# Kernel optimization log

Hardware: AMD Instinct MI355X
Metric: run time of the kernel (lower is better)

## Reference

```python
import jax, jax.numpy as jnp
import numpy as np

B, C, IMG, P = 64, 3, 224, 16
HP = IMG // P                 # 14 patches per side
N = HP * HP                   # 196 patches
R = 196                       # num_superpixels
D, HEADS, DEPTH = 384, 6, 12
HD = D // HEADS
MLP = 4 * D
CLS = 1000
WIN = 4                       # local attention window radius
SEQ = R + 1


def setup_inputs() -> dict:
    key = jax.random.key(0)
    ks = jax.random.split(key, 16)
    nrm = lambda k, s: jax.random.normal(k, s, jnp.float32) * 0.02
    return dict(
        x=jax.random.normal(ks[0], (B, C, IMG, IMG), jnp.float32),
        seg=jax.random.randint(ks[1], (B, IMG, IMG), 0, R, jnp.int32),
        patch_W=nrm(ks[2], (C * P * P, D)), patch_b=jnp.zeros((D,), jnp.float32),
        cls_token=nrm(ks[3], (1, 1, D)),
        pos_W=nrm(ks[4], (2, D)), pos_b=jnp.zeros((D,), jnp.float32),
        cls_pos=nrm(ks[5], (D,)),
        ln1_w=jnp.ones((DEPTH, D), jnp.float32), ln1_b=jnp.zeros((DEPTH, D), jnp.float32),
        qkv_W=nrm(ks[6], (DEPTH, D, 3 * D)), qkv_b=jnp.zeros((DEPTH, 3 * D), jnp.float32),
        proj_W=nrm(ks[7], (DEPTH, D, D)), proj_b=jnp.zeros((DEPTH, D), jnp.float32),
        ln2_w=jnp.ones((DEPTH, D), jnp.float32), ln2_b=jnp.zeros((DEPTH, D), jnp.float32),
        mlp_W1=nrm(ks[8], (DEPTH, D, MLP)), mlp_b1=jnp.zeros((DEPTH, MLP), jnp.float32),
        mlp_W2=nrm(ks[9], (DEPTH, MLP, D)), mlp_b2=jnp.zeros((DEPTH, D), jnp.float32),
        norm_w=jnp.ones((D,), jnp.float32), norm_b=jnp.zeros((D,), jnp.float32),
        head_W=nrm(ks[10], (D, CLS)), head_b=jnp.zeros((CLS,), jnp.float32),
    )


def _ln(x, w, b):
    m = x.mean(-1, keepdims=True)
    v = ((x - m) ** 2).mean(-1, keepdims=True)
    return (x - m) * jax.lax.rsqrt(v + 1e-5) * w + b


def _forward(x, seg, patch_W, patch_b, cls_token, pos_W, pos_b, cls_pos,
             ln1_w, ln1_b, qkv_W, qkv_b, proj_W, proj_b, ln2_w, ln2_b,
             mlp_W1, mlp_b1, mlp_W2, mlp_b2, norm_w, norm_b, head_W, head_b):
    # --- patch embedding (conv stride==kernel == patchify + matmul) -> [B,N,D]
    xp = x.reshape(B, C, HP, P, HP, P).transpose(0, 2, 4, 1, 3, 5).reshape(B, N, C * P * P)
    emb = xp @ patch_W + patch_b
    # --- patch -> superpixel id: segmentation label at patch center pixel
    centers = jnp.arange(HP) * P + P // 2
    patch_seg = seg[:, centers[:, None], centers[None, :]].reshape(B, N)
    # --- mean pooling per superpixel (fused segment reduce over all batches)
    pids = (jnp.arange(B, dtype=patch_seg.dtype)[:, None] * R + patch_seg).reshape(-1)
    sums = jax.ops.segment_sum(emb.reshape(-1, D), pids, num_segments=B * R)
    cnts = jax.ops.segment_sum(jnp.ones((B * N,), emb.dtype), pids, num_segments=B * R)
    pooled = (sums / jnp.maximum(cnts, 1.0)[:, None]).reshape(B, R, D)
    # --- superpixel centroids via pixel-level segment reduce -> [B,R,2] (x,y)
    coords = jnp.arange(IMG, dtype=jnp.float32) / IMG
    yg, xg = jnp.meshgrid(coords, coords, indexing='ij')
    gid = (jnp.arange(B, dtype=seg.dtype)[:, None] * R + seg.reshape(B, -1)).reshape(-1)
    pix = IMG * IMG
    pcnt = jax.ops.segment_sum(jnp.ones((B * pix,), jnp.float32), gid, num_segments=B * R)
    ysum = jax.ops.segment_sum(jnp.broadcast_to(yg.reshape(-1), (B, pix)).reshape(-1), gid, num_segments=B * R)
    xsum = jax.ops.segment_sum(jnp.broadcast_to(xg.reshape(-1), (B, pix)).reshape(-1), gid, num_segments=B * R)
    safe = jnp.maximum(pcnt, 1.0)
    cx = jnp.where(pcnt > 0, xsum / safe, 0.5)
    cy = jnp.where(pcnt > 0, ysum / safe, 0.5)
    centroids = jnp.stack([cx, cy], axis=-1).reshape(B, R, 2)
    # --- prepend cls token, add dynamic (centroid-based) positional encoding
    tok = jnp.concatenate([jnp.broadcast_to(cls_token, (B, 1, D)), pooled], axis=1)
    pos = jnp.concatenate([jnp.broadcast_to(cls_pos[None, None, :], (B, 1, D)),
                           centroids @ pos_W + pos_b], axis=1)
    h = tok + pos
    # --- local (banded) attention mask; cls token attends globally
    idx = jnp.arange(SEQ)
    band = jnp.abs(idx[:, None] - idx[None, :]) <= WIN
    band = band | (idx[:, None] == 0) | (idx[None, :] == 0)
    neg = jnp.float32(-1e9)
    scale = 1.0 / np.sqrt(HD)
    for l in range(DEPTH):
        z = _ln(h, ln1_w[l], ln1_b[l])
        qkv = (z @ qkv_W[l] + qkv_b[l]).reshape(B, SEQ, 3, HEADS, HD)
        q, k, v = qkv[:, :, 0], qkv[:, :, 1], qkv[:, :, 2]
        s = jnp.einsum('bqhd,bkhd->bhqk', q, k) * scale
        s = jnp.where(band[None, None], s, neg)
        a = jax.nn.softmax(s, axis=-1)
        o = jnp.einsum('bhqk,bkhd->bqhd', a, v).reshape(B, SEQ, D)
        h = h + o @ proj_W[l] + proj_b[l]
        z = _ln(h, ln2_w[l], ln2_b[l])
        h = h + jax.nn.gelu(z @ mlp_W1[l] + mlp_b1[l]) @ mlp_W2[l] + mlp_b2[l]
    h = _ln(h, norm_w, norm_b)
    return h[:, 0] @ head_W + head_b


def reference(x, seg, patch_W, patch_b, cls_token, pos_W, pos_b, cls_pos,
              ln1_w, ln1_b, qkv_W, qkv_b, proj_W, proj_b, ln2_w, ln2_b,
              mlp_W1, mlp_b1, mlp_W2, mlp_b2, norm_w, norm_b, head_W, head_b):
    return _forward(x, seg, patch_W, patch_b, cls_token, pos_W, pos_b, cls_pos,
                    ln1_w, ln1_b, qkv_W, qkv_b, proj_W, proj_b, ln2_w, ln2_b,
                    mlp_W1, mlp_b1, mlp_W2, mlp_b2, norm_w, norm_b, head_W, head_b)
```

## Files before the change

### kernel.cpp

```cpp
#include <hip/hip_runtime.h>
#include <hip/hip_bf16.h>
#include <math.h>

typedef unsigned short ushort_t;
typedef unsigned int uint_t;
typedef __attribute__((ext_vector_type(8))) short short8;
typedef __attribute__((ext_vector_type(4))) float f32x4;

#define BATCH 64
#define CHN 3
#define IMG 224
#define PATCH 16
#define HP 14
#define NPATCH 196
#define RSEG 196
#define DMODEL 384
#define HEADS 6
#define HD 64
#define DEPTH 12
#define MLPD 1536
#define CLS 1000
#define WIN 4
#define SEQ 197
#define PIX (IMG*IMG)
#define PATCHK (CHN*PATCH*PATCH)
#define CPARTS 16
#define PPP (PIX / CPARTS)

__device__ __forceinline__ ushort_t f2bf(float f) {
  uint_t u = __float_as_uint(f);
  u += 0x7FFFu + ((u >> 16) & 1u);
  return (ushort_t)(u >> 16);
}
__device__ __forceinline__ float bf2f(ushort_t u) {
  return __uint_as_float((uint_t)u << 16);
}
__device__ __forceinline__ float gelu_tanh(float x) {
  float z = 0.7978845608028654f * (x + 0.044715f * x * x * x);
  z = fminf(fmaxf(z, -15.f), 15.f);
  float t = exp2f(2.8853900817779268f * z);
  return x * t / (t + 1.f);
}
__device__ __forceinline__ int xcd_swizzle(int bid, int nwg) {
  int q = nwg >> 3, r = nwg & 7;
  int xcd = bid & 7, idx = bid >> 3;
  int start = (xcd < r) ? xcd * (q + 1) : r * (q + 1) + (xcd - r) * q;
  return start + idx;
}
__device__ __forceinline__ float dot16bf(const ushort_t* a, const ushort_t* b) {
  const uint_t* a32 = (const uint_t*)a;
  const uint_t* b32 = (const uint_t*)b;
  float acc = 0.f;
#pragma unroll
  for (int w = 0; w < 8; w++) {
    uint_t ka = a32[w], kb = b32[w];
    acc += bf2f((ushort_t)(ka & 0xffff)) * bf2f((ushort_t)(kb & 0xffff));
    acc += bf2f((ushort_t)(ka >> 16)) * bf2f((ushort_t)(kb >> 16));
  }
  return acc;
}

__global__ __launch_bounds__(256) void convtrans_kernel(
    const float* __restrict__ W, ushort_t* __restrict__ Wt, int K, int N) {
  __shared__ float t[32][33];
  int k0 = blockIdx.y * 32, n0 = blockIdx.x * 32;
  const float* Wl = W + (size_t)blockIdx.z * K * N;
  ushort_t* Wtl = Wt + (size_t)blockIdx.z * K * N;
  int tx = threadIdx.x & 31, ty = threadIdx.x >> 5;
#pragma unroll
  for (int i = 0; i < 32; i += 8)
    t[ty + i][tx] = Wl[(size_t)(k0 + ty + i) * N + n0 + tx];
  __syncthreads();
#pragma unroll
  for (int i = 0; i < 32; i += 8)
    Wtl[(size_t)(n0 + ty + i) * K + k0 + tx] = f2bf(t[tx][ty + i]);
}

__global__ __launch_bounds__(256) void patchify_kernel(
    const float* __restrict__ x, ushort_t* __restrict__ xp, int total4) {
  int idx = blockIdx.x * 256 + threadIdx.x;
  if (idx >= total4) return;
  int kq = idx % (PATCHK / 4);
  int m = idx / (PATCHK / 4);
  int n = m % NPATCH;
  int b = m / NPATCH;
  int hi = n / HP, wi = n % HP;
  int k = kq * 4;
  int c = k >> 8;
  int rem = k & 255;
  int pi = rem >> 4, pj = rem & 15;
  int row = hi * PATCH + pi, col = wi * PATCH + pj;
  f32x4 v = *(const f32x4*)&x[(((size_t)b * CHN + c) * IMG + row) * IMG + col];
  uint_t p0 = (uint_t)f2bf(v[0]) | ((uint_t)f2bf(v[1]) << 16);
  uint_t p1 = (uint_t)f2bf(v[2]) | ((uint_t)f2bf(v[3]) << 16);
  uint_t* dst = (uint_t*)(xp + (size_t)idx * 4);
  dst[0] = p0;
  dst[1] = p1;
}

template <int BMT, bool GELU, bool RESID, int OUTMODE>
__global__ __launch_bounds__(256) void gemm_gl(
    const ushort_t* __restrict__ A, const ushort_t* __restrict__ Bt,
    const float* __restrict__ bias, const float* __restrict__ resid,
    void* __restrict__ Cout, int M, int N, int K, int gx) {
  constexpr int AWS = BMT * 2;
  constexpr int AI = AWS / 64;
  constexpr int MF = 4;
  constexpr int NF = (BMT == 128) ? 4 : 2;
  constexpr int BUF_U = (BMT + 128) * 64;
  constexpr int CS_U = BMT * 136;
  constexpr int SMEM_U = (2 * BUF_U > CS_U) ? 2 * BUF_U : CS_U;
  __shared__ __align__(16) ushort_t smem[SMEM_U];
  int tid = threadIdx.x;
  int wave = tid >> 6, lane = tid & 63;
  int flat = xcd_swizzle(blockIdx.x, gridDim.x);
  int bx = flat % gx, by = flat / gx;
  int bm = by * BMT, bn = bx * 128;
  int wr = (BMT == 128) ? (wave >> 1) * 64 : 0;
  int wc = (BMT == 128) ? (wave & 1) * 64 : wave * 32;
  f32x4 acc[MF][NF];
#pragma unroll
  for (int m = 0; m < MF; m++)
#pragma unroll
    for (int n = 0; n < NF; n++)
#pragma unroll
      for (int e = 0; e < 4; e++) acc[m][n][e] = 0.f;

  int r = lane & 15;
  int cfrag = lane >> 4;

  const ushort_t* asrc[AI];
  uint_t adst[AI];
#pragma unroll
  for (int j = 0; j < AI; j++) {
    int s = wave * AWS + j * 64 + lane;
    int row = s >> 3;
    int cp = s & 7;
    int c = cp ^ ((row >> 1) & 7);
    asrc[j] = A + (size_t)(bm + row) * K + c * 8;
    adst[j] = (uint_t)(wave * AWS + j * 64) * 8;
  }
  const ushort_t* bsrc[4];
  uint_t bdst[4];
#pragma unroll
  for (int j = 0; j < 4; j++) {
    int s = wave * 256 + j * 64 + lane;
    int row = s >> 3;
    int cp = s & 7;
    int c = cp ^ ((row >> 1) & 7);
    bsrc[j] = Bt + (size_t)(bn + row) * K + c * 8;
    bdst[j] = (uint_t)(BMT * 64) + (uint_t)(wave * 256 + j * 64) * 8;
  }
  uint_t aoff[2][MF], boff[2][NF];
#pragma unroll
  for (int kk = 0; kk < 2; kk++) {
#pragma unroll
    for (int m = 0; m < MF; m++) {
      int row = wr + m * 16 + r;
      int sl = (kk * 4 + cfrag) ^ ((row >> 1) & 7);
      aoff[kk][m] = (uint_t)(row * 64 + sl * 8);
    }
#pragma unroll
    for (int n = 0; n < NF; n++) {
      int row = wc + n * 16 + r;
      int sl = (kk * 4 + cfrag) ^ ((row >> 1) & 7);
      boff[kk][n] = (uint_t)(BMT * 64 + row * 64 + sl * 8);
    }
  }

  auto STAGE = [&](int buf) {
    ushort_t* base = smem + buf * BUF_U;
#pragma unroll
    for (int j = 0; j < AI; j++)
      __builtin_amdgcn_global_load_lds(
          (const __attribute__((address_space(1))) void*)asrc[j],
          (__attribute__((address_space(3))) void*)(base + adst[j]), 16, 0, 0);
#pragma unroll
    for (int j = 0; j < 4; j++)
      __builtin_amdgcn_global_load_lds(
          (const __attribute__((address_space(1))) void*)bsrc[j],
          (__attribute__((address_space(3))) void*)(base + bdst[j]), 16, 0, 0);
  };
  auto ADVANCE = [&]() {
#pragma unroll
    for (int j = 0; j < AI; j++) asrc[j] += 64;
#pragma unroll
    for (int j = 0; j < 4; j++) bsrc[j] += 64;
  };

  STAGE(0);
  ADVANCE();
  __syncthreads();
  int cur = 0;
  for (int k0 = 0; k0 < K; k0 += 64) {
    if (k0 + 64 < K) {
      STAGE(cur ^ 1);
      ADVANCE();
    }
    ushort_t* base = smem + cur * BUF_U;
#pragma unroll
    for (int kk = 0; kk < 2; kk++) {
      short8 af[MF], bfr[NF];
#pragma unroll
      for (int m = 0; m < MF; m++)
        af[m] = *(const short8*)(base + aoff[kk][m]);
#pragma unroll
      for (int n = 0; n < NF; n++)
        bfr[n] = *(const short8*)(base + boff[kk][n]);
      __builtin_amdgcn_s_setprio(1);
#pragma unroll
      for (int m = 0; m < MF; m++)
#pragma unroll
        for (int n = 0; n < NF; n++)
          acc[m][n] = __builtin_amdgcn_mfma_f32_16x16x32_bf16(
              af[m], bfr[n], acc[m][n], 0, 0, 0);
      __builtin_amdgcn_s_setprio(0);
    }
    __syncthreads();
    cur ^= 1;
  }
  int q4 = (lane >> 4) * 4;
  if (OUTMODE == 0) {
#pragma unroll
    for (int n = 0; n < NF; n++) {
      int col = bn + wc + n * 16 + r;
      float bi = bias[col];
#pragma unroll
      for (int m = 0; m < MF; m++) {
#pragma unroll
        for (int e = 0; e < 4; e++) {
          int row = bm + wr + m * 16 + q4 + e;
          if (row < M) {
            float v = acc[m][n][e] + bi;
            if (GELU) v = gelu_tanh(v);
            if (RESID) v += resid[(size_t)row * N + col];
            ((float*)Cout)[(size_t)row * N + col] = v;
          }
        }
      }
    }
  } else {
    ushort_t* Cs = smem;
#pragma unroll
    for (int n = 0; n < NF; n++) {
      int lc = wc + n * 16 + r;
      float bi = bias[bn + lc];
#pragma unroll
      for (int m = 0; m < MF; m++) {
#pragma unroll
        for (int e = 0; e < 4; e++) {
          int lr = wr + m * 16 + q4 + e;
          float v = acc[m][n][e] + bi;
          if (GELU) v = gelu_tanh(v);
          if (RESID) v += resid[(size_t)(bm + lr) * N + bn + lc];
          Cs[lr * 136 + lc] = f2bf(v);
        }
      }
    }
    __syncthreads();
    constexpr int CHUNKS = BMT * 16;
#pragma unroll
    for (int c = 0; c < CHUNKS / 256; c++) {
      int id = c * 256 + tid;
      int row = id >> 4, ch = id & 15;
      int grow = bm + row;
      if (grow < M) {
        short8 val = *(const short8*)(Cs + row * 136 + ch * 8);
        int gcol = bn + ch * 8;
        if (OUTMODE == 1) {
          *(short8*)((ushort_t*)Cout + (size_t)grow * N + gcol) = val;
        } else {
          int b_ = grow / SEQ, t_ = grow - b_ * SEQ;
          int which = gcol / DMODEL;
          int hcol = gcol - which * DMODEL;
          int hh = hcol >> 6, d0 = hcol & 63;
          *(short8*)((ushort_t*)Cout +
                     ((((size_t)b_ * 3 + which) * HEADS + hh) * SEQ + t_) * 64 +
                     d0) = val;
        }
      }
    }
  }
}

__global__ __launch_bounds__(256) void zeroacc_kernel(int* __restrict__ g,
                                                      int n) {
  int i = blockIdx.x * 256 + threadIdx.x;
  if (i < n) g[i] = 0;
}

__global__ __launch_bounds__(256) void centroid_part_kernel(
    const int* __restrict__ seg, int* __restrict__ gacc) {
  __shared__ int cnt[RSEG], si[RSEG], sj[RSEG];
  int b = blockIdx.x, part = blockIdx.y, tid = threadIdx.x;
  for (int r = tid; r < RSEG; r += 256) { cnt[r] = 0; si[r] = 0; sj[r] = 0; }
  __syncthreads();
  const int* s = seg + (size_t)b * PIX;
  int p0 = part * PPP;
  for (int p = p0 + tid; p < p0 + PPP; p += 256) {
    int r = s[p];
    int i = p / IMG, j = p % IMG;
    atomicAdd(&cnt[r], 1);
    atomicAdd(&si[r], i);
    atomicAdd(&sj[r], j);
  }
  __syncthreads();
  for (int r = tid; r < RSEG; r += 256) {
    int c = cnt[r];
    if (c | si[r] | sj[r]) {
      int* g = gacc + ((size_t)b * RSEG + r) * 3;
      atomicAdd(&g[0], c);
      atomicAdd(&g[1], si[r]);
      atomicAdd(&g[2], sj[r]);
    }
  }
}
__global__ __launch_bounds__(256) void centroid_fin_kernel(
    const int* __restrict__ gacc, float* __restrict__ cent) {
  int b = blockIdx.x, tid = threadIdx.x;
  for (int r = tid; r < RSEG; r += 256) {
    const int* g = gacc + ((size_t)b * RSEG + r) * 3;
    int c = g[0];
    float cx = 0.5f, cy = 0.5f;
    if (c > 0) {
      cx = ((float)g[2] / (float)IMG) / (float)c;
      cy = ((float)g[1] / (float)IMG) / (float)c;
    }
    cent[((size_t)b * RSEG + r) * 2 + 0] = cx;
    cent[((size_t)b * RSEG + r) * 2 + 1] = cy;
  }
}

__global__ __launch_bounds__(256) void patchseg_kernel(
    const int* __restrict__ seg, int* __restrict__ pseg) {
  int idx = blockIdx.x * 256 + threadIdx.x;
  if (idx >= BATCH * NPATCH) return;
  int n = idx % NPATCH, b = idx / NPATCH;
  int hi = n / HP, wi = n % HP;
  pseg[idx] = seg[(size_t)b * PIX + (8 + hi * PATCH) * IMG + (8 + wi * PATCH)];
}

__global__ __launch_bounds__(64) void buildlists_kernel(
    const int* __restrict__ pseg, int* __restrict__ starts,
    int* __restrict__ lists) {
  __shared__ int cnt[RSEG];
  int b = blockIdx.x;
  if (threadIdx.x != 0) return;
  const int* ps = pseg + b * NPATCH;
  for (int r = 0; r < RSEG; r++) cnt[r] = 0;
  for (int n = 0; n < NPATCH; n++) cnt[ps[n]]++;
  int run = 0;
  int* st = starts + b * (RSEG + 1);
  for (int r = 0; r < RSEG; r++) {
    st[r] = run;
    int c = cnt[r];
    cnt[r] = run;
    run += c;
  }
  st[RSEG] = run;
  int* li = lists + b * NPATCH;
  for (int n = 0; n < NPATCH; n++) {
    int r = ps[n];
    li[cnt[r]++] = n;
  }
}

__global__ __launch_bounds__(384) void pool_assemble_kernel(
    const float* __restrict__ emb, const float* __restrict__ cent,
    const int* __restrict__ starts, const int* __restrict__ lists,
    const float* __restrict__ cls_token, const float* __restrict__ cls_pos,
    const float* __restrict__ pos_W, const float* __restrict__ pos_b,
    float* __restrict__ h) {
  int t = blockIdx.x;
  int b = t / SEQ, s = t % SEQ;
  int d = threadIdx.x;
  float out;
  if (s == 0) {
    out = cls_token[d] + cls_pos[d];
  } else {
    int r = s - 1;
    int st = starts[b * (RSEG + 1) + r];
    int en = starts[b * (RSEG + 1) + r + 1];
    float acc = 0.f;
    for (int i = st; i < en; i++) {
      int n = lists[b * NPATCH + i];
      acc += emb[((size_t)b * NPATCH + n) * DMODEL + d];
    }
    int cnt = en - st;
    float pooled = acc / (float)(cnt > 0 ? cnt : 1);
    float cx = cent[((size_t)b * RSEG + r) * 2 + 0];
    float cy = cent[((size_t)b * RSEG + r) * 2 + 1];
    out = pooled + cx * pos_W[d] + cy * pos_W[DMODEL + d] + pos_b[d];
  }
  h[(size_t)t * DMODEL + d] = out;
}

template <bool OUTBF16>
__global__ __launch_bounds__(256) void ln_kernel(
    const float* __restrict__ in, void* __restrict__ out,
    const float* __restrict__ w, const float* __restrict__ b, int inStride) {
  int wave = threadIdx.x >> 6, lane = threadIdx.x & 63;
  int row = blockIdx.x * 4 + wave;
  const float* xr = in + (size_t)row * inStride;
  float2 v0 = *(const float2*)(xr + lane * 2);
  float2 v1 = *(const float2*)(xr + 128 + lane * 2);
  float2 v2 = *(const float2*)(xr + 256 + lane * 2);
  float s = v0.x + v0.y + v1.x + v1.y + v2.x + v2.y;
  float s2 = v0.x * v0.x + v0.y * v0.y + v1.x * v1.x + v1.y * v1.y +
             v2.x * v2.x + v2.y * v2.y;
#pragma unroll
  for (int off = 32; off; off >>= 1) {
    s += __shfl_xor(s, off);
    s2 += __shfl_xor(s2, off);
  }
  float m = s / (float)DMODEL;
  float var = s2 / (float)DMODEL - m * m;
  float rs = rsqrtf(var + 1e-5f);
#pragma unroll
  for (int i = 0; i < 3; i++) {
    int d0 = i * 128 + lane * 2;
    float x0 = (i == 0) ? v0.x : (i == 1) ? v1.x : v2.x;
    float x1 = (i == 0) ? v0.y : (i == 1) ? v1.y : v2.y;
    float o0 = (x0 - m) * rs * w[d0] + b[d0];
    float o1 = (x1 - m) * rs * w[d0 + 1] + b[d0 + 1];
    if (OUTBF16) {
      uint_t pack = (uint_t)f2bf(o0) | ((uint_t)f2bf(o1) << 16);
      *(uint_t*)((ushort_t*)out + (size_t)row * DMODEL + d0) = pack;
    } else {
      float2 pk = {o0, o1};
      *(float2*)((float*)out + (size_t)row * DMODEL + d0) = pk;
    }
  }
}

__global__ __launch_bounds__(256) void attn_kernel(
    const ushort_t* __restrict__ qkvp, ushort_t* __restrict__ o) {
  int wave = threadIdx.x >> 6, lane = threadIdx.x & 63;
  int gi = blockIdx.x * 4 + wave;
  int hh = blockIdx.y, b = blockIdx.z;
  const size_t hstride = (size_t)HEADS * SEQ * 64;
  size_t base0 = ((size_t)b * 3 * HEADS + hh) * SEQ * 64;
  const ushort_t* Qh = qkvp + base0;
  const ushort_t* Kh = qkvp + base0 + hstride;
  const ushort_t* Vh = qkvp + base0 + 2 * hstride;
  if (gi < 49) {
    int q0 = 1 + gi * 4;
    int base = q0 - 4;
    if (base < 1) base = 1;
    int row = lane >> 2, dq = lane & 3;
    int key = (row == 0) ? 0 : base + row - 1;
    bool rowvalid = (key <= 196);
    int kaddr = rowvalid ? key : 196;
    const uint_t* kp = (const uint_t*)(Kh + (size_t)kaddr * 64 + dq * 16);
    uint_t kf[8];
#pragma unroll
    for (int w = 0; w < 8; w++) kf[w] = kp[w];
    float v[16];
#pragma unroll
    for (int r = 0; r < 16; r++) {
      int kr = (r == 0) ? 0 : base + r - 1;
      if (kr > 196) kr = 196;
      v[r] = bf2f(Vh[(size_t)kr * 64 + lane]);
    }
#pragma unroll
    for (int i = 0; i < 4; i++) {
      int qi = q0 + i;
      const uint_t* qp = (const uint_t*)(Qh + (size_t)qi * 64 + dq * 16);
      float part = 0.f;
#pragma unroll
      for (int w = 0; w < 8; w++) {
        uint_t ka = kf[w], qa = qp[w];
        part += bf2f((ushort_t)(ka & 0xffff)) * bf2f((ushort_t)(qa & 0xffff));
        part += bf2f((ushort_t)(ka >> 16)) * bf2f((ushort_t)(qa >> 16));
      }
      part += __shfl_xor(part, 1);
      part += __shfl_xor(part, 2);
      int lo = qi - WIN;
      if (lo < 1) lo = 1;
      int hi = qi + WIN;
      if (hi > 196) hi = 196;
      bool valid = rowvalid && ((key == 0) || (key >= lo && key <= hi));
      float s = valid ? part * 0.125f : -1e30f;
      float mx = s;
      mx = fmaxf(mx, __shfl_xor(mx, 4));
      mx = fmaxf(mx, __shfl_xor(mx, 8));
      mx = fmaxf(mx, __shfl_xor(mx, 16));
      mx = fmaxf(mx, __shfl_xor(mx, 32));
      float p = valid ? expf(s - mx) : 0.f;
      float sum = p;
      sum += __shfl_xor(sum, 4);
      sum += __shfl_xor(sum, 8);
      sum += __shfl_xor(sum, 16);
      sum += __shfl_xor(sum, 32);
      float acc = 0.f;
#pragma unroll
      for (int r = 0; r < 16; r++) acc += __shfl(p, r * 4) * v[r];
      o[((size_t)(b * SEQ + qi)) * DMODEL + hh * HD + lane] = f2bf(acc / sum);
    }
  } else if (gi == 49) {
    const ushort_t* qr = Qh;
    float sc0 = -1e30f, sc1 = -1e30f, sc2 = -1e30f, sc3 = -1e30f;
#pragma unroll
    for (int c = 0; c < 4; c++) {
      int key = c * 64 + lane;
      float s = -1e30f;
      if (key < SEQ) {
        const ushort_t* kr = Kh + (size_t)key * 64;
        float acc = dot16bf(kr, qr) + dot16bf(kr + 16, qr + 16) +
                    dot16bf(kr + 32, qr + 32) + dot16bf(kr + 48, qr + 48);
        s = acc * 0.125f;
      }
      if (c == 0) sc0 = s; else if (c == 1) sc1 = s; else if (c == 2) sc2 = s; else sc3 = s;
    }
    float mx = fmaxf(fmaxf(sc0, sc1), fmaxf(sc2, sc3));
#pragma unroll
    for (int off = 32; off; off >>= 1) mx = fmaxf(mx, __shfl_xor(mx, off));
    float p0 = expf(sc0 - mx), p1 = expf(sc1 - mx);
    float p2 = expf(sc2 - mx), p3 = expf(sc3 - mx);
    float sum = p0 + p1 + p2 + p3;
#pragma unroll
    for (int off = 32; off; off >>= 1) sum += __shfl_xor(sum, off);
    float acc = 0.f;
#pragma unroll
    for (int c = 0; c < 4; c++) {
      float pc = (c == 0) ? p0 : (c == 1) ? p1 : (c == 2) ? p2 : p3;
      int jmax = (c < 3) ? 64 : (SEQ - 192);
      for (int jj = 0; jj < jmax; ++jj) {
        float pt = __shfl(pc, jj);
        acc += pt * bf2f(Vh[(size_t)(c * 64 + jj) * 64 + lane]);
      }
    }
    o[((size_t)(b * SEQ)) * DMODEL + hh * HD + lane] = f2bf(acc / sum);
  }
}

__global__ __launch_bounds__(256) void head_kernel(
    const float* __restrict__ hn, const float* __restrict__ W,
    const float* __restrict__ bias, float* __restrict__ out) {
  __shared__ float hs[DMODEL];
  int b = blockIdx.y;
  int c = blockIdx.x * 256 + threadIdx.x;
  for (int d = threadIdx.x; d < DMODEL; d += 256)
    hs[d] = hn[(size_t)b * DMODEL + d];
  __syncthreads();
  if (c >= CLS) return;
  float acc = bias[c];
  for (int d = 0; d < DMODEL; d++) acc += hs[d] * W[(size_t)d * CLS + c];
  out[(size_t)b * CLS + c] = acc;
}

extern "C" void kernel_launch(void* const* d_in, const int* in_sizes, int n_in,
                              void* d_out, int out_size, void* d_ws,
                              size_t ws_size, hipStream_t stream) {
  const float* x = (const float*)d_in[0];
  const int* seg = (const int*)d_in[1];
  const float* patch_W = (const float*)d_in[2];
  const float* patch_b = (const float*)d_in[3];
  const float* cls_token = (const float*)d_in[4];
  const float* pos_W = (const float*)d_in[5];
  const float* pos_b = (const float*)d_in[6];
  const float* cls_pos = (const float*)d_in[7];
  const float* ln1_w = (const float*)d_in[8];
  const float* ln1_b = (const float*)d_in[9];
  const float* qkv_W = (const float*)d_in[10];
  const float* qkv_b = (const float*)d_in[11];
  const float* proj_W = (const float*)d_in[12];
  const float* proj_b = (const float*)d_in[13];
  const float* ln2_w = (const float*)d_in[14];
  const float* ln2_b = (const float*)d_in[15];
  const float* mlp_W1 = (const float*)d_in[16];
  const float* mlp_b1 = (const float*)d_in[17];
  const float* mlp_W2 = (const float*)d_in[18];
  const float* mlp_b2 = (const float*)d_in[19];
  const float* norm_w = (const float*)d_in[20];
  const float* norm_b = (const float*)d_in[21];
  const float* head_W = (const float*)d_in[22];
  const float* head_b = (const float*)d_in[23];
  float* out = (float*)d_out;

  const int M0 = BATCH * NPATCH;
  const int MT = BATCH * SEQ;

  char* ws = (char*)d_ws;
  size_t off = 0;
  auto alloc = [&](size_t bytes) { char* p = ws + off; off += (bytes + 255) & ~(size_t)255; return p; };
  ushort_t* patch_Wt = (ushort_t*)alloc((size_t)PATCHK * DMODEL * 2);
  ushort_t* qkv_Wt   = (ushort_t*)alloc((size_t)DEPTH * DMODEL * 3 * DMODEL * 2);
  ushort_t* proj_Wt  = (ushort_t*)alloc((size_t)DEPTH * DMODEL * DMODEL * 2);
  ushort_t* mlp1_Wt  = (ushort_t*)alloc((size_t)DEPTH * DMODEL * MLPD * 2);
  ushort_t* mlp2_Wt  = (ushort_t*)alloc((size_t)DEPTH * MLPD * DMODEL * 2);
  char* big = alloc((size_t)MT * MLPD * 2);
  ushort_t* xp_bf = (ushort_t*)big;
  ushort_t* mlph_bf = (ushort_t*)big;
  ushort_t* qkvb = (ushort_t*)alloc((size_t)MT * 3 * DMODEL * 2);
  char* eo = alloc((size_t)M0 * DMODEL * 4);
  float* emb = (float*)eo;
  ushort_t* attno = (ushort_t*)eo;
  float* h = (float*)alloc((size_t)MT * DMODEL * 4);
  ushort_t* z_bf = (ushort_t*)alloc((size_t)MT * DMODEL * 2);
  float* cent = (float*)alloc((size_t)BATCH * RSEG * 2 * 4);
  float* hn = (float*)alloc((size_t)BATCH * DMODEL * 4);
  int* pseg = (int*)alloc((size_t)BATCH * NPATCH * 4);
  int* starts = (int*)alloc((size_t)BATCH * (RSEG + 1) * 4);
  int* lists = (int*)alloc((size_t)BATCH * NPATCH * 4);
  int* gacc = (int*)alloc((size_t)BATCH * RSEG * 3 * 4);

  convtrans_kernel<<<dim3(DMODEL / 32, PATCHK / 32, 1), 256, 0, stream>>>(
      patch_W, patch_Wt, PATCHK, DMODEL);
  convtrans_kernel<<<dim3(3 * DMODEL / 32, DMODEL / 32, DEPTH), 256, 0, stream>>>(
      qkv_W, qkv_Wt, DMODEL, 3 * DMODEL);
  convtrans_kernel<<<dim3(DMODEL / 32, DMODEL / 32, DEPTH), 256, 0, stream>>>(
      proj_W, proj_Wt, DMODEL, DMODEL);
  convtrans_kernel<<<dim3(MLPD / 32, DMODEL / 32, DEPTH), 256, 0, stream>>>(
      mlp_W1, mlp1_Wt, DMODEL, MLPD);
  convtrans_kernel<<<dim3(DMODEL / 32, MLPD / 32, DEPTH), 256, 0, stream>>>(
      mlp_W2, mlp2_Wt, MLPD, DMODEL);

  {
    int total4 = M0 * PATCHK / 4;
    patchify_kernel<<<(total4 + 255) / 256, 256, 0, stream>>>(x, xp_bf, total4);
  }
  gemm_gl<64, false, false, 0><<<(DMODEL / 128) * (M0 / 64), 256, 0, stream>>>(
      xp_bf, patch_Wt, patch_b, nullptr, emb, M0, DMODEL, PATCHK, DMODEL / 128);
  {
    int n = BATCH * RSEG * 3;
    zeroacc_kernel<<<(n + 255) / 256, 256, 0, stream>>>(gacc, n);
  }
  centroid_part_kernel<<<dim3(BATCH, CPARTS), 256, 0, stream>>>(seg, gacc);
  centroid_fin_kernel<<<BATCH, 256, 0, stream>>>(gacc, cent);
  patchseg_kernel<<<(M0 + 255) / 256, 256, 0, stream>>>(seg, pseg);
  buildlists_kernel<<<BATCH, 64, 0, stream>>>(pseg, starts, lists);
  pool_assemble_kernel<<<MT, 384, 0, stream>>>(emb, cent, starts, lists,
                                               cls_token, cls_pos, pos_W,
                                               pos_b, h);

  int gy128 = (MT + 127) / 128;
  int gy64 = MT / 64;
  for (int l = 0; l < DEPTH; l++) {
    ln_kernel<true><<<MT / 4, 256, 0, stream>>>(h, z_bf, ln1_w + l * DMODEL,
                                                ln1_b + l * DMODEL, DMODEL);
    gemm_gl<128, false, false, 2><<<(3 * DMODEL / 128) * gy128, 256, 0, stream>>>(
        z_bf, qkv_Wt + (size_t)l * DMODEL * 3 * DMODEL, qkv_b + l * 3 * DMODEL,
        nullptr, qkvb, MT, 3 * DMODEL, DMODEL, 3 * DMODEL / 128);
    attn_kernel<<<dim3(13, HEADS, BATCH), 256, 0, stream>>>(qkvb, attno);
    gemm_gl<64, false, true, 0><<<(DMODEL / 128) * gy64, 256, 0, stream>>>(
        attno, proj_Wt + (size_t)l * DMODEL * DMODEL, proj_b + l * DMODEL, h,
        h, MT, DMODEL, DMODEL, DMODEL / 128);
    ln_kernel<true><<<MT / 4, 256, 0, stream>>>(h, z_bf, ln2_w + l * DMODEL,
                                                ln2_b + l * DMODEL, DMODEL);
    gemm_gl<128, true, false, 1><<<(MLPD / 128) * gy128, 256, 0, stream>>>(
        z_bf, mlp1_Wt + (size_t)l * DMODEL * MLPD, mlp_b1 + l * MLPD, nullptr,
        mlph_bf, MT, MLPD, DMODEL, MLPD / 128);
    gemm_gl<64, false, true, 0><<<(DMODEL / 128) * gy64, 256, 0, stream>>>(
        mlph_bf, mlp2_Wt + (size_t)l * MLPD * DMODEL, mlp_b2 + l * DMODEL, h,
        h, MT, DMODEL, MLPD, DMODEL / 128);
  }
  ln_kernel<false><<<BATCH / 4, 256, 0, stream>>>(h, hn, norm_w, norm_b,
                                                  SEQ * DMODEL);
  head_kernel<<<dim3((CLS + 255) / 256, BATCH), 256, 0, stream>>>(
      hn, head_W, head_b, out);
}
```

Baseline: 1.925 ms.

## Fuse MLP up-projection, GELU and down-projection into one kernel

Replaces the two tiled MLP GEMM launches with a single kernel. Each block takes 16 rows, computes the 1536-wide hidden activation with GELU into shared memory as bf16, then multiplies it by W2 and adds the result into the residual. This removes the global write and read of the large hidden tensor. In exchange, the new kernel loads weights directly from global memory without LDS tiling, and every 16-row block re-reads the full W1 and W2, which greatly increases weight traffic and lowers MFMA data reuse.

```diff
diff --git a/kernel.cpp b/kernel.cpp
--- a/kernel.cpp
+++ b/kernel.cpp
@@ -26,6 +26,7 @@
 #define PATCHK (CHN*PATCH*PATCH)
 #define CPARTS 16
 #define PPP (PIX / CPARTS)
+#define HIDP 1544
 
 __device__ __forceinline__ ushort_t f2bf(float f) {
   uint_t u = __float_as_uint(f);
@@ -279,6 +280,69 @@
                      d0) = val;
         }
       }
+    }
+  }
+}
+
+__global__ __launch_bounds__(256) void fused_mlp_kernel(
+    const ushort_t* __restrict__ z, const ushort_t* __restrict__ W1t,
+    const float* __restrict__ b1, const ushort_t* __restrict__ W2t,
+    const float* __restrict__ b2, float* __restrict__ h) {
+  __shared__ __align__(16) ushort_t hid[16 * HIDP];
+  int tid = threadIdx.x;
+  int wave = tid >> 6, lane = tid & 63;
+  int bm = (int)blockIdx.x * 16;
+  int r = lane & 15;
+  int koff = (lane >> 4) * 8;
+  int q4 = (lane >> 4) * 4;
+
+  for (int nch = 0; nch < 12; nch++) {
+    int colbase = nch * 128 + wave * 32;
+    f32x4 acc0 = {0.f, 0.f, 0.f, 0.f};
+    f32x4 acc1 = {0.f, 0.f, 0.f, 0.f};
+#pragma unroll
+    for (int ks = 0; ks < 12; ks++) {
+      short8 a = *(const short8*)(z + (size_t)(bm + r) * DMODEL + ks * 32 + koff);
+      short8 w0 = *(const short8*)(W1t + (size_t)(colbase + r) * DMODEL + ks * 32 + koff);
+      short8 w1 = *(const short8*)(W1t + (size_t)(colbase + 16 + r) * DMODEL + ks * 32 + koff);
+      acc0 = __builtin_amdgcn_mfma_f32_16x16x32_bf16(a, w0, acc0, 0, 0, 0);
+      acc1 = __builtin_amdgcn_mfma_f32_16x16x32_bf16(a, w1, acc1, 0, 0, 0);
+    }
+    int c0 = colbase + r, c1 = colbase + 16 + r;
+    float bi0 = b1[c0], bi1 = b1[c1];
+#pragma unroll
+    for (int e = 0; e < 4; e++) {
+      int row = q4 + e;
+      hid[row * HIDP + c0] = f2bf(gelu_tanh(acc0[e] + bi0));
+      hid[row * HIDP + c1] = f2bf(gelu_tanh(acc1[e] + bi1));
+    }
+  }
+  __syncthreads();
+
+  int cbase = wave * 96;
+  f32x4 acc[6];
+#pragma unroll
+  for (int f = 0; f < 6; f++)
+#pragma unroll
+    for (int e = 0; e < 4; e++) acc[f][e] = 0.f;
+  for (int ks = 0; ks < 48; ks++) {
+    short8 a = *(const short8*)(hid + r * HIDP + ks * 32 + koff);
+#pragma unroll
+    for (int f = 0; f < 6; f++) {
+      short8 w = *(const short8*)(W2t + (size_t)(cbase + f * 16 + r) * MLPD +
+                                  ks * 32 + koff);
+      acc[f] = __builtin_amdgcn_mfma_f32_16x16x32_bf16(a, w, acc[f], 0, 0, 0);
+    }
+  }
+#pragma unroll
+  for (int f = 0; f < 6; f++) {
+    int col = cbase + f * 16 + r;
+    float bi = b2[col];
+#pragma unroll
+    for (int e = 0; e < 4; e++) {
+      int row = bm + q4 + e;
+      float* hp = h + (size_t)row * DMODEL + col;
+      *hp = *hp + acc[f][e] + bi;
     }
   }
 }
@@ -591,7 +655,6 @@
   ushort_t* mlp2_Wt  = (ushort_t*)alloc((size_t)DEPTH * MLPD * DMODEL * 2);
   char* big = alloc((size_t)MT * MLPD * 2);
   ushort_t* xp_bf = (ushort_t*)big;
-  ushort_t* mlph_bf = (ushort_t*)big;
   ushort_t* qkvb = (ushort_t*)alloc((size_t)MT * 3 * DMODEL * 2);
   char* eo = alloc((size_t)M0 * DMODEL * 4);
   float* emb = (float*)eo;
@@ -648,12 +711,9 @@
         h, MT, DMODEL, DMODEL, DMODEL / 128);
     ln_kernel<true><<<MT / 4, 256, 0, stream>>>(h, z_bf, ln2_w + l * DMODEL,
                                                 ln2_b + l * DMODEL, DMODEL);
-    gemm_gl<128, true, false, 1><<<(MLPD / 128) * gy128, 256, 0, stream>>>(
-        z_bf, mlp1_Wt + (size_t)l * DMODEL * MLPD, mlp_b1 + l * MLPD, nullptr,
-        mlph_bf, MT, MLPD, DMODEL, MLPD / 128);
-    gemm_gl<64, false, true, 0><<<(DMODEL / 128) * gy64, 256, 0, stream>>>(
-        mlph_bf, mlp2_Wt + (size_t)l * MLPD * DMODEL, mlp_b2 + l * DMODEL, h,
-        h, MT, DMODEL, MLPD, DMODEL / 128);
+    fused_mlp_kernel<<<MT / 16, 256, 0, stream>>>(
+        z_bf, mlp1_Wt + (size_t)l * DMODEL * MLPD, mlp_b1 + l * MLPD,
+        mlp2_Wt + (size_t)l * MLPD * DMODEL, mlp_b2 + l * DMODEL, h);
   }
   ln_kernel<false><<<BATCH / 4, 256, 0, stream>>>(h, hn, norm_w, norm_b,
                                                   SEQ * DMODEL);
```

New measurement: 4.313 ms. 2.24x slower.
